# Performance work log

Hardware: AMD Instinct MI355X
Metric: run time of the kernel (lower is better)

Reference implementation:

```python
import jax, jax.numpy as jnp
import numpy as np


def setup_inputs() -> dict:
    key = jax.random.key(0)
    k1, k2 = jax.random.split(key)
    D = 512
    B, N = 32, 512
    panel_embeddings = jax.random.normal(k1, (B, N, D), dtype=jnp.float32)
    # nn.Bilinear(D, D, 1) weight: (1, D, D) -> squeeze to (D, D); bias: scalar
    bound = 1.0 / np.sqrt(D)
    W = jax.random.uniform(k2, (D, D), dtype=jnp.float32, minval=-bound, maxval=bound)
    b = jnp.float32(0.0)
    return {"panel_embeddings": panel_embeddings, "W": W, "b": b}


def reference(panel_embeddings, W, b):
    # score[b,i,j] = x_i^T W x_j + b, with diagonal forced to 0 (loop skips i==j)
    xw = jnp.einsum('bid,de->bie', panel_embeddings, W)          # (B, N, D)
    scores = jnp.einsum('bie,bje->bij', xw, panel_embeddings) + b  # (B, N, N)
    N = panel_embeddings.shape[1]
    mask = ~jnp.eye(N, dtype=bool)
    return jnp.where(mask, scores, jnp.zeros_like(scores))
```

## Files before the change

### kernel.cpp

```cpp
#include <hip/hip_runtime.h>
#include <stdint.h>

#define BATCH 32
#define NDIM 512
#define DDIM 512
#define XELEMS (BATCH * NDIM * DDIM)
#define WELEMS (DDIM * DDIM)

typedef _Float16 f16x8 __attribute__((ext_vector_type(8)));
typedef _Float16 f16x4v __attribute__((ext_vector_type(4)));
typedef float f32x4 __attribute__((ext_vector_type(4)));

__device__ __forceinline__ void gl_lds16(const _Float16* g, _Float16* l) {
    __builtin_amdgcn_global_load_lds(
        (const __attribute__((address_space(1))) unsigned int*)(g),
        (__attribute__((address_space(3))) unsigned int*)(l),
        16, 0, 0);
}

__global__ __launch_bounds__(256) void prep(const float4* __restrict__ X4,
                                            f16x4v* __restrict__ Xh4,
                                            const float* __restrict__ W,
                                            _Float16* __restrict__ Wt) {
    __shared__ float tile[32][33];
    int bid = blockIdx.x;
    if (bid < XELEMS / 4 / 256) {
        int i = bid * 256 + threadIdx.x;
        float4 v = X4[i];
        f16x4v o;
        o.x = (_Float16)v.x;
        o.y = (_Float16)v.y;
        o.z = (_Float16)v.z;
        o.w = (_Float16)v.w;
        Xh4[i] = o;
    } else {
        int t = bid - XELEMS / 4 / 256;
        int bx = t & 15;
        int by = t >> 4;
        int tx = threadIdx.x & 31;
        int ty = threadIdx.x >> 5;
        for (int r = ty; r < 32; r += 8)
            tile[r][tx] = W[(by * 32 + r) * DDIM + bx * 32 + tx];
        __syncthreads();
        for (int r = ty; r < 32; r += 8)
            Wt[(size_t)(bx * 32 + r) * DDIM + by * 32 + tx] = (_Float16)tile[tx][r];
    }
}

template <int EPI>
__global__ __launch_bounds__(256) void gemm_bt(const _Float16* __restrict__ A,
                                               const _Float16* __restrict__ Bt,
                                               _Float16* __restrict__ Yout,
                                               float* __restrict__ Sout,
                                               const float* __restrict__ bias_ptr) {
    __shared__ __align__(16) _Float16 As[128 * 64];
    __shared__ __align__(16) _Float16 Bs[128 * 64];

    const int tid  = threadIdx.x;
    const int lane = tid & 63;
    const int wv   = tid >> 6;

    const int m0 = blockIdx.y * 128;
    const int n0 = blockIdx.x * 128;
    const int batch = blockIdx.z;

    const _Float16* Ab = A;
    const _Float16* Bb = Bt;
    if (EPI == 1) {
        Ab = A  + (size_t)batch * (NDIM * DDIM);
        Bb = Bt + (size_t)batch * (NDIM * DDIM);
    }

    const int lr = lane >> 3;
    const int lc = lane & 7;
    const int lk = ((lc ^ lr) * 8);

    const int quad = lane >> 4;
    const int l16  = lane & 15;

    f32x4 acc[2][8];
#pragma unroll
    for (int i = 0; i < 2; ++i)
#pragma unroll
        for (int j = 0; j < 8; ++j)
            acc[i][j] = (f32x4){0.f, 0.f, 0.f, 0.f};

    for (int k0 = 0; k0 < DDIM; k0 += 64) {
#pragma unroll
        for (int t = 0; t < 4; ++t) {
            int chunk = wv * 4 + t;
            int row   = chunk * 8 + lr;
            gl_lds16(Ab + (size_t)(m0 + row) * DDIM + k0 + lk, &As[chunk * 512]);
            gl_lds16(Bb + (size_t)(n0 + row) * DDIM + k0 + lk, &Bs[chunk * 512]);
        }
        __syncthreads();

#pragma unroll
        for (int kkc = 0; kkc < 8; kkc += 4) {
            const int pa = (((kkc + quad) ^ (l16 & 7)) * 8);
            f16x8 a0 = *(const f16x8*)&As[(wv * 32 +      l16) * 64 + pa];
            f16x8 a1 = *(const f16x8*)&As[(wv * 32 + 16 + l16) * 64 + pa];
#pragma unroll
            for (int nt = 0; nt < 8; ++nt) {
                f16x8 b = *(const f16x8*)&Bs[(nt * 16 + l16) * 64 + pa];
                acc[0][nt] = __builtin_amdgcn_mfma_f32_16x16x32_f16(a0, b, acc[0][nt], 0, 0, 0);
                acc[1][nt] = __builtin_amdgcn_mfma_f32_16x16x32_f16(a1, b, acc[1][nt], 0, 0, 0);
            }
        }
        __syncthreads();
    }

    float bias = (EPI == 1) ? bias_ptr[0] : 0.f;
#pragma unroll
    for (int mt = 0; mt < 2; ++mt) {
#pragma unroll
        for (int nt = 0; nt < 8; ++nt) {
#pragma unroll
            for (int r = 0; r < 4; ++r) {
                int gi = m0 + wv * 32 + mt * 16 + quad * 4 + r;
                int gj = n0 + nt * 16 + l16;
                float v = acc[mt][nt][r];
                if (EPI == 0) {
                    Yout[(size_t)gi * DDIM + gj] = (_Float16)v;
                } else {
                    v += bias;
                    if (gi == gj) v = 0.f;
                    Sout[((size_t)batch * NDIM + gi) * NDIM + gj] = v;
                }
            }
        }
    }
}

extern "C" void kernel_launch(void* const* d_in, const int* in_sizes, int n_in,
                              void* d_out, int out_size, void* d_ws, size_t ws_size,
                              hipStream_t stream) {
    const float* X  = (const float*)d_in[0];
    const float* W  = (const float*)d_in[1];
    const float* bp = (const float*)d_in[2];
    float* out = (float*)d_out;

    _Float16* Xh = (_Float16*)d_ws;
    _Float16* Wt = Xh + XELEMS;
    _Float16* Y  = Wt + WELEMS;

    prep<<<XELEMS / 4 / 256 + 256, 256, 0, stream>>>((const float4*)X, (f16x4v*)Xh, W, Wt);

    gemm_bt<0><<<dim3(4, 128, 1), 256, 0, stream>>>(Xh, Wt, Y, nullptr, nullptr);

    gemm_bt<1><<<dim3(4, 4, BATCH), 256, 0, stream>>>(Y, Xh, nullptr, out, bp);

    (void)in_sizes; (void)n_in; (void)out_size; (void)ws_size;
}
```

Baseline: 119.6 us.

## Double-buffer LDS tiles in GEMM and remap grid to 1D block order

Adds a two-stage LDS ping-pong so the next K-slice's global-to-LDS loads are issued before computing on the current slice, removing one barrier per iteration. It also flattens the launch grid and changes block-to-tile mapping, so consecutive blocks share the same B tile (first GEMM) or differ by batch (second GEMM). The cost is doubled LDS use per block (64KB), which may reduce occupancy.

```diff
diff --git a/kernel.cpp b/kernel.cpp
--- a/kernel.cpp
+++ b/kernel.cpp
@@ -6,6 +6,7 @@
 #define DDIM 512
 #define XELEMS (BATCH * NDIM * DDIM)
 #define WELEMS (DDIM * DDIM)
+#define KITERS (DDIM / 64)
 
 typedef _Float16 f16x8 __attribute__((ext_vector_type(8)));
 typedef _Float16 f16x4v __attribute__((ext_vector_type(4)));
@@ -53,16 +54,26 @@
                                                _Float16* __restrict__ Yout,
                                                float* __restrict__ Sout,
                                                const float* __restrict__ bias_ptr) {
-    __shared__ __align__(16) _Float16 As[128 * 64];
-    __shared__ __align__(16) _Float16 Bs[128 * 64];
+    __shared__ __align__(16) _Float16 As[2][128 * 64];
+    __shared__ __align__(16) _Float16 Bs[2][128 * 64];
 
     const int tid  = threadIdx.x;
     const int lane = tid & 63;
     const int wv   = tid >> 6;
 
-    const int m0 = blockIdx.y * 128;
-    const int n0 = blockIdx.x * 128;
-    const int batch = blockIdx.z;
+    int m0, n0, batch;
+    if (EPI == 0) {
+        int blk = blockIdx.x;
+        n0 = (blk >> 7) * 128;
+        m0 = (blk & 127) * 128;
+        batch = 0;
+    } else {
+        int blk = blockIdx.x;
+        batch = blk & 31;
+        int t = blk >> 5;
+        n0 = (t & 3) * 128;
+        m0 = (t >> 2) * 128;
+    }
 
     const _Float16* Ab = A;
     const _Float16* Bb = Bt;
@@ -75,6 +86,16 @@
     const int lc = lane & 7;
     const int lk = ((lc ^ lr) * 8);
 
+    const _Float16* ga[4];
+    const _Float16* gb[4];
+#pragma unroll
+    for (int t = 0; t < 4; ++t) {
+        int chunk = wv * 4 + t;
+        int row   = chunk * 8 + lr;
+        ga[t] = Ab + (size_t)(m0 + row) * DDIM + lk;
+        gb[t] = Bb + (size_t)(n0 + row) * DDIM + lk;
+    }
+
     const int quad = lane >> 4;
     const int l16  = lane & 15;
 
@@ -85,29 +106,39 @@
         for (int j = 0; j < 8; ++j)
             acc[i][j] = (f32x4){0.f, 0.f, 0.f, 0.f};
 
-    for (int k0 = 0; k0 < DDIM; k0 += 64) {
 #pragma unroll
-        for (int t = 0; t < 4; ++t) {
-            int chunk = wv * 4 + t;
-            int row   = chunk * 8 + lr;
-            gl_lds16(Ab + (size_t)(m0 + row) * DDIM + k0 + lk, &As[chunk * 512]);
-            gl_lds16(Bb + (size_t)(n0 + row) * DDIM + k0 + lk, &Bs[chunk * 512]);
+    for (int t = 0; t < 4; ++t) {
+        int chunk = wv * 4 + t;
+        gl_lds16(ga[t], &As[0][chunk * 512]);
+        gl_lds16(gb[t], &Bs[0][chunk * 512]);
+    }
+
+    for (int it = 0; it < KITERS; ++it) {
+        const int buf = it & 1;
+        __syncthreads();
+
+        if (it + 1 < KITERS) {
+            const int k1 = (it + 1) * 64;
+#pragma unroll
+            for (int t = 0; t < 4; ++t) {
+                int chunk = wv * 4 + t;
+                gl_lds16(ga[t] + k1, &As[buf ^ 1][chunk * 512]);
+                gl_lds16(gb[t] + k1, &Bs[buf ^ 1][chunk * 512]);
+            }
         }
-        __syncthreads();
 
 #pragma unroll
         for (int kkc = 0; kkc < 8; kkc += 4) {
             const int pa = (((kkc + quad) ^ (l16 & 7)) * 8);
-            f16x8 a0 = *(const f16x8*)&As[(wv * 32 +      l16) * 64 + pa];
-            f16x8 a1 = *(const f16x8*)&As[(wv * 32 + 16 + l16) * 64 + pa];
+            f16x8 a0 = *(const f16x8*)&As[buf][(wv * 32 +      l16) * 64 + pa];
+            f16x8 a1 = *(const f16x8*)&As[buf][(wv * 32 + 16 + l16) * 64 + pa];
 #pragma unroll
             for (int nt = 0; nt < 8; ++nt) {
-                f16x8 b = *(const f16x8*)&Bs[(nt * 16 + l16) * 64 + pa];
+                f16x8 b = *(const f16x8*)&Bs[buf][(nt * 16 + l16) * 64 + pa];
                 acc[0][nt] = __builtin_amdgcn_mfma_f32_16x16x32_f16(a0, b, acc[0][nt], 0, 0, 0);
                 acc[1][nt] = __builtin_amdgcn_mfma_f32_16x16x32_f16(a1, b, acc[1][nt], 0, 0, 0);
             }
         }
-        __syncthreads();
     }
 
     float bias = (EPI == 1) ? bias_ptr[0] : 0.f;
@@ -146,9 +177,9 @@
 
     prep<<<XELEMS / 4 / 256 + 256, 256, 0, stream>>>((const float4*)X, (f16x4v*)Xh, W, Wt);
 
-    gemm_bt<0><<<dim3(4, 128, 1), 256, 0, stream>>>(Xh, Wt, Y, nullptr, nullptr);
+    gemm_bt<0><<<512, 256, 0, stream>>>(Xh, Wt, Y, nullptr, nullptr);
 
-    gemm_bt<1><<<dim3(4, 4, BATCH), 256, 0, stream>>>(Y, Xh, nullptr, out, bp);
+    gemm_bt<1><<<512, 256, 0, stream>>>(Y, Xh, nullptr, out, bp);
 
     (void)in_sizes; (void)n_in; (void)out_size; (void)ws_size;
 }
```

After: 115.4 us. 1.04x faster.
